# Kernel tuning notes

Measured on AMD Instinct MI355X. Metric: run time of the kernel, lower is better.

The kernel has to match this reference:

```python
import jax, jax.numpy as jnp
import numpy as np

N_NODES = 100000
N_EDGES = 1600000
D_IN = 128
D_HID = 128
D_OUT = 128
N_GRAPHS = 64


def setup_inputs() -> dict:
    key = jax.random.key(0)
    ks = jax.random.split(key, 10)
    x = jax.random.normal(ks[0], (N_NODES, D_IN), dtype=jnp.float32)
    edge_index = jax.random.randint(ks[1], (2, N_EDGES), 0, N_NODES, dtype=jnp.int64)
    graph_id = jnp.sort(jax.random.randint(ks[2], (N_NODES,), 0, N_GRAPHS, dtype=jnp.int64))
    s1 = 1.0 / np.sqrt(D_IN)
    s2 = 1.0 / np.sqrt(D_HID)
    s3 = 1.0 / np.sqrt(D_OUT)
    W1 = jax.random.normal(ks[3], (D_IN, D_HID), dtype=jnp.float32) * s1
    b1 = jnp.zeros((D_HID,), dtype=jnp.float32)
    W2 = jax.random.normal(ks[4], (D_HID, D_OUT), dtype=jnp.float32) * s2
    b2 = jnp.zeros((D_OUT,), dtype=jnp.float32)
    Wr1 = jax.random.normal(ks[5], (D_OUT, D_OUT), dtype=jnp.float32) * s3
    br1 = jnp.zeros((D_OUT,), dtype=jnp.float32)
    Wr2 = jax.random.normal(ks[6], (D_OUT, D_OUT), dtype=jnp.float32) * s3
    br2 = jnp.zeros((D_OUT,), dtype=jnp.float32)
    return {"x": x, "edge_index": edge_index, "graph_id": graph_id,
            "num_graphs": N_GRAPHS, "W1": W1, "b1": b1, "W2": W2, "b2": b2,
            "Wr1": Wr1, "br1": br1, "Wr2": Wr2, "br2": br2}


def _graph_conv(h, W, b, src, dst, norm_src, norm_dst, n_nodes):
    # DGL GraphConv, norm='both': out = D_dst^{-1/2} A (D_src^{-1/2} h) W + b
    h = h * norm_src[:, None]
    h = h @ W  # project first (cheap, keeps SpMM on the smaller/equal dim)
    agg = jax.ops.segment_sum(h[src], dst, num_segments=n_nodes)
    return agg * norm_dst[:, None] + b


def reference(x, edge_index, graph_id, num_graphs, W1, b1, W2, b2, Wr1, br1, Wr2, br2):
    src, dst = edge_index[0], edge_index[1]
    n_nodes = x.shape[0]
    ones = jnp.ones((src.shape[0],), dtype=x.dtype)
    deg_out = jax.ops.segment_sum(ones, src, num_segments=n_nodes)
    deg_in = jax.ops.segment_sum(ones, dst, num_segments=n_nodes)
    norm_src = jnp.clip(deg_out, 1.0) ** -0.5
    norm_dst = jnp.clip(deg_in, 1.0) ** -0.5

    # layer 1 + relu (dropout is identity in eval mode)
    h = _graph_conv(x, W1, b1, src, dst, norm_src, norm_dst, n_nodes)
    h = jax.nn.relu(h)
    # layer 2 + relu
    h = _graph_conv(h, W2, b2, src, dst, norm_src, norm_dst, n_nodes)
    h = jax.nn.relu(h)

    # per-graph mean pooling (dgl.mean_nodes)
    sums = jax.ops.segment_sum(h, graph_id, num_segments=num_graphs)
    counts = jax.ops.segment_sum(jnp.ones((n_nodes,), dtype=h.dtype), graph_id,
                                 num_segments=num_graphs)
    hg = sums / jnp.clip(counts, 1.0)[:, None]

    # readout MLP: Linear -> ReLU -> Linear
    out = jax.nn.relu(hg @ Wr1 + br1) @ Wr2 + br2
    return (out, h)
```

## Files before the change

### kernel.cpp

```cpp
#include <hip/hip_runtime.h>
#include <math.h>


#define D 128
#define BSH 8
#define BKT 256
#define CAP 4608
#define SCHUNK 3200

typedef _Float16 half8 __attribute__((ext_vector_type(8)));
typedef _Float16 half4v __attribute__((ext_vector_type(4)));
typedef _Float16 half2v __attribute__((ext_vector_type(2)));
typedef float f32x4 __attribute__((ext_vector_type(4)));

union H8 { half8 v; half2v h[4]; };

__global__ __launch_bounds__(512) void k_build(const int* __restrict__ src,
                                               const int* __restrict__ dst,
                                               int* __restrict__ cnt_d,
                                               int* __restrict__ cnt_s,
                                               int* __restrict__ packed_d,
                                               unsigned char* __restrict__ packed_s8,
                                               const float* __restrict__ W1,
                                               const float* __restrict__ W2,
                                               _Float16* __restrict__ Wt1,
                                               _Float16* __restrict__ Wt2,
                                               const int* __restrict__ gid,
                                               int* __restrict__ gptr,
                                               int N, int E, int nbkt) {
  __shared__ int hd[512], hs[512], exd[512], exs[512], based[512], bases[512];
  __shared__ int sd[SCHUNK];
  __shared__ unsigned char ss[SCHUNK];
  const int t = threadIdx.x;
  const int bid = blockIdx.x;

  for (int idx = bid * 512 + t; idx < 2 * 128 * 128; idx += gridDim.x * 512) {
    int m = idx >> 14, i = idx & 16383;
    int k = i >> 7, n = i & 127;
    (m ? Wt2 : Wt1)[n * 128 + k] = (_Float16)((m ? W2 : W1)[i]);
  }
  if (bid == gridDim.x - 1 && t <= 64) {
    int lo = 0, hi = N;
    while (lo < hi) {
      int m = (lo + hi) >> 1;
      if (gid[m] < t) lo = m + 1; else hi = m;
    }
    gptr[t] = lo;
  }

  hd[t] = 0; hs[t] = 0;
  __syncthreads();
  const int chunk = (E + gridDim.x - 1) / gridDim.x;
  const int lo = bid * chunk, hi = min(lo + chunk, E);
  const int n = hi - lo;
  for (int i = lo + t; i < hi; i += 512) {
    atomicAdd(&hd[dst[i] >> BSH], 1);
    atomicAdd(&hs[src[i] >> BSH], 1);
  }
  __syncthreads();
  int cD = hd[t], cS = hs[t];
  for (int off = 1; off < 512; off <<= 1) {
    int ad = (t >= off) ? hd[t - off] : 0;
    int as = (t >= off) ? hs[t - off] : 0;
    __syncthreads();
    hd[t] += ad; hs[t] += as;
    __syncthreads();
  }
  exd[t] = hd[t] - cD;
  exs[t] = hs[t] - cS;
  if (t < nbkt) {
    based[t] = cD ? atomicAdd(&cnt_d[t], cD) : 0;
    bases[t] = cS ? atomicAdd(&cnt_s[t], cS) : 0;
  }
  __syncthreads();
  hd[t] = 0; hs[t] = 0;
  __syncthreads();
  for (int i = lo + t; i < hi; i += 512) {
    int s = src[i], d = dst[i];
    int b1 = d >> BSH;
    int r1 = atomicAdd(&hd[b1], 1);
    sd[exd[b1] + r1] = ((d & (BKT - 1)) << 17) | s;
    int b2 = s >> BSH;
    int r2 = atomicAdd(&hs[b2], 1);
    ss[exs[b2] + r2] = (unsigned char)(s & (BKT - 1));
  }
  __syncthreads();
  for (int i = t; i < n; i += 512) {
    int blo = 0, bhi = nbkt - 1;
    while (blo < bhi) {
      int m = (blo + bhi + 1) >> 1;
      if (exd[m] <= i) blo = m; else bhi = m - 1;
    }
    int p = based[blo] + (i - exd[blo]);
    if (p < CAP) packed_d[blo * CAP + p] = sd[i];
    blo = 0; bhi = nbkt - 1;
    while (blo < bhi) {
      int m = (blo + bhi + 1) >> 1;
      if (exs[m] <= i) blo = m; else bhi = m - 1;
    }
    p = bases[blo] + (i - exs[blo]);
    if (p < CAP) packed_s8[blo * CAP + p] = ss[i];
  }
}

union FineLds {
  struct { int excl[256]; int ecache[CAP]; int sorted[CAP]; } d;
  struct { _Float16 As[64][136]; _Float16 Cs[64][128]; } s;
};

__global__ __launch_bounds__(512) void k_fine(const int* __restrict__ packed_d,
                                              const int* __restrict__ cnt_d,
                                              int* __restrict__ row_lo,
                                              int* __restrict__ row_hi,
                                              int* __restrict__ csr,
                                              const unsigned char* __restrict__ packed_s8,
                                              const int* __restrict__ cnt_s,
                                              float* __restrict__ norm_src,
                                              const float* __restrict__ x,
                                              const _Float16* __restrict__ Wt1,
                                              _Float16* __restrict__ P,
                                              int N, int nbkt) {
  __shared__ int hist[256];
  __shared__ FineLds u;
  int t = threadIdx.x;
  if (blockIdx.x >= nbkt) {
    int b = blockIdx.x - nbkt;
    size_t lo = (size_t)b * CAP;
    int cnt = min(cnt_s[b], CAP);
    if (t < 256) hist[t] = 0;
    __syncthreads();
    for (int e = t; e < cnt; e += 512)
      atomicAdd(&hist[packed_s8[lo + e]], 1);
    __syncthreads();
    int nbase = b << BSH;
    if (t < 256 && nbase + t < N)
      norm_src[nbase + t] = rsqrtf(fmaxf((float)hist[t], 1.0f));
    __syncthreads();
    const int l = t & 63;
    const int c = l & 15, quad = l >> 4;
    const int w = t >> 6;
    const int strip = w & 3, chalf = w >> 2;
    for (int ti = 0; ti < 4; ++ti) {
      const int r0 = nbase + ti * 64;
      for (int i = t; i < 64 * 32; i += 512) {
        int r = i >> 5, c4 = i & 31;
        float4 v = {0.f, 0.f, 0.f, 0.f};
        if (r0 + r < N) {
          v = ((const float4*)x)[(size_t)(r0 + r) * 32 + c4];
          float s = rsqrtf(fmaxf((float)hist[ti * 64 + r], 1.0f));
          v.x *= s; v.y *= s; v.z *= s; v.w *= s;
        }
        half4v h = {(_Float16)v.x, (_Float16)v.y, (_Float16)v.z, (_Float16)v.w};
        *(half4v*)&u.s.As[r][c4 * 4] = h;
      }
      __syncthreads();
      f32x4 acc[4];
#pragma unroll
      for (int nt = 0; nt < 4; ++nt) acc[nt] = (f32x4){0.f, 0.f, 0.f, 0.f};
#pragma unroll
      for (int kc = 0; kc < 4; ++kc) {
        half8 a = *(const half8*)&u.s.As[strip * 16 + c][kc * 32 + quad * 8];
#pragma unroll
        for (int nt = 0; nt < 4; ++nt) {
          half8 bb = *(const half8*)&Wt1[(size_t)(chalf * 64 + nt * 16 + c) * 128 + kc * 32 + quad * 8];
          acc[nt] = __builtin_amdgcn_mfma_f32_16x16x32_f16(a, bb, acc[nt], 0, 0, 0);
        }
      }
#pragma unroll
      for (int nt = 0; nt < 4; ++nt)
#pragma unroll
        for (int r = 0; r < 4; ++r)
          u.s.Cs[strip * 16 + quad * 4 + r][chalf * 64 + nt * 16 + c] = (_Float16)acc[nt][r];
      __syncthreads();
      for (int i = t; i < 64 * 16; i += 512) {
        int r = i >> 4, c8 = i & 15;
        if (r0 + r < N)
          ((half8*)P)[(size_t)(r0 + r) * 16 + c8] = *(half8*)&u.s.Cs[r][c8 * 8];
      }
      __syncthreads();
    }
    return;
  }
  int b = blockIdx.x;
  int lo = b * CAP;
  int cnt = min(cnt_d[b], CAP);
  if (t < 256) hist[t] = 0;
  __syncthreads();
  for (int e = t; e < cnt; e += 512) {
    int p = packed_d[lo + e];
    u.d.ecache[e] = p;
    atomicAdd(&hist[p >> 17], 1);
  }
  __syncthreads();
  int v = (t < 256) ? hist[t] : 0;
  for (int off = 1; off < 256; off <<= 1) {
    int a = (t >= off && t < 256) ? hist[t - off] : 0;
    __syncthreads();
    if (t < 256) hist[t] += a;
    __syncthreads();
  }
  int nbase = b << BSH;
  if (t < 256) {
    u.d.excl[t] = hist[t] - v;
    if (nbase + t < N) {
      row_lo[nbase + t] = lo + hist[t] - v;
      row_hi[nbase + t] = lo + hist[t];
    }
  }
  __syncthreads();
  if (t < 256) hist[t] = 0;
  __syncthreads();
  for (int e = t; e < cnt; e += 512) {
    int p = u.d.ecache[e];
    int dlow = p >> 17;
    int r = atomicAdd(&hist[dlow], 1);
    u.d.sorted[u.d.excl[dlow] + r] = p & 0x1FFFF;
  }
  __syncthreads();
  for (int e = t; e < cnt; e += 512)
    csr[lo + e] = u.d.sorted[e];
}

__global__ __launch_bounds__(256) void k_gemm2(const _Float16* __restrict__ A,
                                               const _Float16* __restrict__ Wt,
                                               _Float16* __restrict__ C, int N) {
  __shared__ _Float16 As[64][136];
  __shared__ _Float16 Cs[64][128];
  const int r0 = blockIdx.x * 64;
  const int t = threadIdx.x;
  for (int i = t; i < 64 * 16; i += 256) {
    int r = i >> 4, c8 = i & 15;
    half8 v = {0, 0, 0, 0, 0, 0, 0, 0};
    if (r0 + r < N) v = ((const half8*)A)[(size_t)(r0 + r) * 16 + c8];
    *(half8*)&As[r][c8 * 8] = v;
  }
  __syncthreads();
  const int w = t >> 6, l = t & 63;
  const int c = l & 15, quad = l >> 4;
  f32x4 acc[8];
#pragma unroll
  for (int nt = 0; nt < 8; ++nt) acc[nt] = (f32x4){0.f, 0.f, 0.f, 0.f};
#pragma unroll
  for (int kc = 0; kc < 4; ++kc) {
    half8 a = *(const half8*)&As[w * 16 + c][kc * 32 + quad * 8];
#pragma unroll
    for (int nt = 0; nt < 8; ++nt) {
      half8 b = *(const half8*)&Wt[(size_t)(nt * 16 + c) * 128 + kc * 32 + quad * 8];
      acc[nt] = __builtin_amdgcn_mfma_f32_16x16x32_f16(a, b, acc[nt], 0, 0, 0);
    }
  }
#pragma unroll
  for (int nt = 0; nt < 8; ++nt)
#pragma unroll
    for (int r = 0; r < 4; ++r)
      Cs[w * 16 + quad * 4 + r][nt * 16 + c] = (_Float16)acc[nt][r];
  __syncthreads();
  for (int i = t; i < 64 * 16; i += 256) {
    int r = i >> 4, c8 = i & 15;
    if (r0 + r < N)
      ((half8*)C)[(size_t)(r0 + r) * 16 + c8] = *(half8*)&Cs[r][c8 * 8];
  }
}

#define PK_ROW(u)                                                           \
  _Pragma("unroll")                                                         \
  for (int k = 0; k < 4; ++k) acch[k] += (u).h[k];

__device__ __forceinline__ void gather_core(const half8* __restrict__ P8,
                                            const int* __restrict__ csr,
                                            int start, int end, int cg, int eg,
                                            int lane, float* acc) {
  half2v acch[4] = {{(_Float16)0.f, (_Float16)0.f}, {(_Float16)0.f, (_Float16)0.f},
                    {(_Float16)0.f, (_Float16)0.f}, {(_Float16)0.f, (_Float16)0.f}};
  for (int s0 = start; s0 < end; s0 += 64) {
    int cnt = min(64, end - s0);
    int idx = (s0 + lane < end) ? csr[s0 + lane] : 0;
    int base = 0;
    for (; base + 16 <= cnt; base += 16) {
      int i0 = __shfl(idx, base + eg);
      int i1 = __shfl(idx, base + 4 + eg);
      int i2 = __shfl(idx, base + 8 + eg);
      int i3 = __shfl(idx, base + 12 + eg);
      H8 u0, u1, u2, u3;
      u0.v = P8[(size_t)i0 * 16 + cg];
      u1.v = P8[(size_t)i1 * 16 + cg];
      u2.v = P8[(size_t)i2 * 16 + cg];
      u3.v = P8[(size_t)i3 * 16 + cg];
      PK_ROW(u0) PK_ROW(u1) PK_ROW(u2) PK_ROW(u3)
    }
    for (; base + 4 <= cnt; base += 4) {
      int i0 = __shfl(idx, base + eg);
      H8 u0;
      u0.v = P8[(size_t)i0 * 16 + cg];
      PK_ROW(u0)
    }
    if (base < cnt) {
      int j = min(base + eg, cnt - 1);
      int i0 = __shfl(idx, j);
      if (base + eg < cnt) {
        H8 u0;
        u0.v = P8[(size_t)i0 * 16 + cg];
        PK_ROW(u0)
      }
    }
  }
#pragma unroll
  for (int k = 0; k < 4; ++k) {
    acc[2 * k]     = (float)acch[k].x;
    acc[2 * k + 1] = (float)acch[k].y;
  }
#pragma unroll
  for (int j = 0; j < 8; ++j) {
    acc[j] += __shfl_xor(acc[j], 16);
    acc[j] += __shfl_xor(acc[j], 32);
  }
}

__global__ __launch_bounds__(256) void k_gather1(const half8* __restrict__ P8,
                                                 const int* __restrict__ row_lo,
                                                 const int* __restrict__ row_hi,
                                                 const int* __restrict__ csr,
                                                 const float* __restrict__ bias,
                                                 const float* __restrict__ norm_src,
                                                 half2v* __restrict__ outH, int N) {
  int wid = (blockIdx.x * 256 + threadIdx.x) >> 6;
  if (wid >= N) return;
  int lane = threadIdx.x & 63;
  int cg = lane & 15, eg = lane >> 4;
  int start = row_lo[wid], end = row_hi[wid];
  float acc[8];
  gather_core(P8, csr, start, end, cg, eg, lane, acc);
  float nd = rsqrtf(fmaxf((float)(end - start), 1.0f));
  float ns = norm_src[wid];
  float2 b = ((const float2*)bias)[cg * 4 + eg];
  half2v o = {(_Float16)(fmaxf(acc[eg * 2] * nd + b.x, 0.f) * ns),
              (_Float16)(fmaxf(acc[eg * 2 + 1] * nd + b.y, 0.f) * ns)};
  outH[(size_t)wid * 64 + cg * 4 + eg] = o;
}

__global__ __launch_bounds__(256) void k_gather2(const half8* __restrict__ P8,
                                                 const int* __restrict__ row_lo,
                                                 const int* __restrict__ row_hi,
                                                 const int* __restrict__ csr,
                                                 const float* __restrict__ bias,
                                                 float2* __restrict__ outH, int N) {
  int wid = (blockIdx.x * 256 + threadIdx.x) >> 6;
  if (wid >= N) return;
  int lane = threadIdx.x & 63;
  int cg = lane & 15, eg = lane >> 4;
  int start = row_lo[wid], end = row_hi[wid];
  float acc[8];
  gather_core(P8, csr, start, end, cg, eg, lane, acc);
  float nd = rsqrtf(fmaxf((float)(end - start), 1.0f));
  float2 b = ((const float2*)bias)[cg * 4 + eg];
  float2 o;
  o.x = fmaxf(acc[eg * 2] * nd + b.x, 0.f);
  o.y = fmaxf(acc[eg * 2 + 1] * nd + b.y, 0.f);
  outH[(size_t)wid * 64 + cg * 4 + eg] = o;
}

__global__ __launch_bounds__(256) void k_pool(const float* __restrict__ H,
                                              const int* __restrict__ gptr,
                                              float* __restrict__ pool) {
  int g = blockIdx.x >> 3, chunk = blockIdx.x & 7;
  int col = threadIdx.x & 127, rpar = threadIdx.x >> 7;
  int s = gptr[g], e = gptr[g + 1];
  float acc = 0.0f;
  for (int r = s + chunk * 2 + rpar; r < e; r += 16)
    acc += H[(size_t)r * D + col];
  __shared__ float red[256];
  red[threadIdx.x] = acc;
  __syncthreads();
  if (rpar == 0) atomicAdd(&pool[g * D + col], acc + red[threadIdx.x + 128]);
}

__global__ __launch_bounds__(128) void k_readout(const float* __restrict__ pool,
                                                 const int* __restrict__ gptr,
                                                 const float* __restrict__ Wr1,
                                                 const float* __restrict__ br1,
                                                 const float* __restrict__ Wr2,
                                                 const float* __restrict__ br2,
                                                 float* __restrict__ out) {
  int g = blockIdx.x;
  int j = threadIdx.x;
  __shared__ float hg[D];
  __shared__ float t1[D];
  float cnt = fmaxf((float)(gptr[g + 1] - gptr[g]), 1.0f);
  hg[j] = pool[(size_t)g * D + j] / cnt;
  __syncthreads();
  float a = br1[j];
  for (int k = 0; k < D; ++k) a += hg[k] * Wr1[(size_t)k * D + j];
  t1[j] = fmaxf(a, 0.0f);
  __syncthreads();
  float b = br2[j];
  for (int k = 0; k < D; ++k) b += t1[k] * Wr2[(size_t)k * D + j];
  out[(size_t)g * D + j] = b;
}

extern "C" void kernel_launch(void* const* d_in, const int* in_sizes, int n_in,
                              void* d_out, int out_size, void* d_ws, size_t ws_size,
                              hipStream_t stream) {
  const float* x   = (const float*)d_in[0];
  const int* edge  = (const int*)d_in[1];
  const int* gid   = (const int*)d_in[2];
  const float* W1  = (const float*)d_in[4];
  const float* b1  = (const float*)d_in[5];
  const float* W2  = (const float*)d_in[6];
  const float* b2  = (const float*)d_in[7];
  const float* Wr1 = (const float*)d_in[8];
  const float* br1 = (const float*)d_in[9];
  const float* Wr2 = (const float*)d_in[10];
  const float* br2 = (const float*)d_in[11];

  const int N = in_sizes[0] / D;
  const int E = in_sizes[1] / 2;
  const int* src = edge;
  const int* dst = edge + E;
  const int nbkt = (N + BKT - 1) >> BSH;

  float* bufA     = (float*)d_ws;
  float* bufB     = bufA + (size_t)N * D;
  int* row_lo     = (int*)(bufB + (size_t)N * D);
  int* row_hi     = row_lo + N;
  int* csr        = row_hi + N;
  float* norm_src = (float*)(csr + (size_t)nbkt * CAP);
  float* pool     = norm_src + N;
  int* gptr       = (int*)(pool + 64 * D);
  int* cnt_d      = gptr + 65;
  int* cnt_s      = cnt_d + 512;
  _Float16* Wt1   = (_Float16*)(cnt_s + 512);
  _Float16* Wt2   = Wt1 + 128 * 128;
  int* packed_d   = (int*)(bufA + (size_t)N * D / 2);
  unsigned char* packed_s8 = (unsigned char*)(packed_d + (size_t)nbkt * CAP);
  size_t need = ((size_t)2 * N * D + 3 * (size_t)N + (size_t)nbkt * CAP
                 + 64 * D + 65 + 1024 + 16384 + 1024) * sizeof(float);
  if (ws_size < need) return;

  float* out_g = (float*)d_out;
  float* h_out = out_g + 64 * D;

  _Float16* P   = (_Float16*)bufA;
  _Float16* h1p = (_Float16*)bufB;

  hipMemsetAsync(pool, 0, (64 * D + 65 + 1024) * sizeof(float), stream);

  const int build_grid = (E + SCHUNK - 1) / SCHUNK;
  k_build<<<build_grid, 512, 0, stream>>>(src, dst, cnt_d, cnt_s,
                                          packed_d, packed_s8,
                                          W1, W2, Wt1, Wt2, gid, gptr,
                                          N, E, nbkt);
  k_fine<<<2 * nbkt, 512, 0, stream>>>(packed_d, cnt_d, row_lo, row_hi, csr,
                                       packed_s8, cnt_s, norm_src,
                                       x, Wt1, P, N, nbkt);

  k_gather1<<<(N * 64 + 255) / 256, 256, 0, stream>>>(
      (const half8*)P, row_lo, row_hi, csr, b1, norm_src, (half2v*)h1p, N);

  const int gemm_grid = (N + 63) / 64;
  k_gemm2<<<gemm_grid, 256, 0, stream>>>(h1p, Wt2, P, N);
  k_gather2<<<(N * 64 + 255) / 256, 256, 0, stream>>>(
      (const half8*)P, row_lo, row_hi, csr, b2, (float2*)h_out, N);

  k_pool<<<64 * 8, 256, 0, stream>>>(h_out, gptr, pool);
  k_readout<<<64, 128, 0, stream>>>(pool, gptr, Wr1, br1, Wr2, br2, out_g);
}
```

Measured before the change: 372.7 us.

## Fuse layer-1 gather with layer-2 GEMM into one kernel via shared memory

Merges the layer-1 SpMM gather kernel and the layer-2 dense projection GEMM. Each block gathers 32 rows (8 rows per wave, run one after another) into LDS and then multiplies them by W2 with MFMA, writing P2 directly. This removes the h1 round trip through global memory and one kernel launch. In exchange, each wave now handles 8 rows serially, and blocks holding high-degree rows are held back at the barrier, which can lower memory-level parallelism in the gather.

```diff
diff --git a/kernel.cpp b/kernel.cpp
--- a/kernel.cpp
+++ b/kernel.cpp
@@ -219,47 +219,6 @@
   __syncthreads();
   for (int e = t; e < cnt; e += 512)
     csr[lo + e] = u.d.sorted[e];
-}
-
-__global__ __launch_bounds__(256) void k_gemm2(const _Float16* __restrict__ A,
-                                               const _Float16* __restrict__ Wt,
-                                               _Float16* __restrict__ C, int N) {
-  __shared__ _Float16 As[64][136];
-  __shared__ _Float16 Cs[64][128];
-  const int r0 = blockIdx.x * 64;
-  const int t = threadIdx.x;
-  for (int i = t; i < 64 * 16; i += 256) {
-    int r = i >> 4, c8 = i & 15;
-    half8 v = {0, 0, 0, 0, 0, 0, 0, 0};
-    if (r0 + r < N) v = ((const half8*)A)[(size_t)(r0 + r) * 16 + c8];
-    *(half8*)&As[r][c8 * 8] = v;
-  }
-  __syncthreads();
-  const int w = t >> 6, l = t & 63;
-  const int c = l & 15, quad = l >> 4;
-  f32x4 acc[8];
-#pragma unroll
-  for (int nt = 0; nt < 8; ++nt) acc[nt] = (f32x4){0.f, 0.f, 0.f, 0.f};
-#pragma unroll
-  for (int kc = 0; kc < 4; ++kc) {
-    half8 a = *(const half8*)&As[w * 16 + c][kc * 32 + quad * 8];
-#pragma unroll
-    for (int nt = 0; nt < 8; ++nt) {
-      half8 b = *(const half8*)&Wt[(size_t)(nt * 16 + c) * 128 + kc * 32 + quad * 8];
-      acc[nt] = __builtin_amdgcn_mfma_f32_16x16x32_f16(a, b, acc[nt], 0, 0, 0);
-    }
-  }
-#pragma unroll
-  for (int nt = 0; nt < 8; ++nt)
-#pragma unroll
-    for (int r = 0; r < 4; ++r)
-      Cs[w * 16 + quad * 4 + r][nt * 16 + c] = (_Float16)acc[nt][r];
-  __syncthreads();
-  for (int i = t; i < 64 * 16; i += 256) {
-    int r = i >> 4, c8 = i & 15;
-    if (r0 + r < N)
-      ((half8*)C)[(size_t)(r0 + r) * 16 + c8] = *(half8*)&Cs[r][c8 * 8];
-  }
 }
 
 #define PK_ROW(u)                                                           \
@@ -316,26 +275,62 @@
   }
 }
 
-__global__ __launch_bounds__(256) void k_gather1(const half8* __restrict__ P8,
-                                                 const int* __restrict__ row_lo,
-                                                 const int* __restrict__ row_hi,
-                                                 const int* __restrict__ csr,
-                                                 const float* __restrict__ bias,
-                                                 const float* __restrict__ norm_src,
-                                                 half2v* __restrict__ outH, int N) {
-  int wid = (blockIdx.x * 256 + threadIdx.x) >> 6;
-  if (wid >= N) return;
-  int lane = threadIdx.x & 63;
-  int cg = lane & 15, eg = lane >> 4;
-  int start = row_lo[wid], end = row_hi[wid];
-  float acc[8];
-  gather_core(P8, csr, start, end, cg, eg, lane, acc);
-  float nd = rsqrtf(fmaxf((float)(end - start), 1.0f));
-  float ns = norm_src[wid];
+__global__ __launch_bounds__(256) void k_g1g2(const half8* __restrict__ P8,
+                                              const int* __restrict__ row_lo,
+                                              const int* __restrict__ row_hi,
+                                              const int* __restrict__ csr,
+                                              const float* __restrict__ bias,
+                                              const float* __restrict__ norm_src,
+                                              const _Float16* __restrict__ Wt2,
+                                              _Float16* __restrict__ P2, int N) {
+  __shared__ _Float16 As[32][136];
+  __shared__ _Float16 Cs[32][128];
+  const int t = threadIdx.x;
+  const int w = t >> 6, lane = t & 63;
+  const int cg = lane & 15, eg = lane >> 4;
+  const int r0 = blockIdx.x * 32;
   float2 b = ((const float2*)bias)[cg * 4 + eg];
-  half2v o = {(_Float16)(fmaxf(acc[eg * 2] * nd + b.x, 0.f) * ns),
-              (_Float16)(fmaxf(acc[eg * 2 + 1] * nd + b.y, 0.f) * ns)};
-  outH[(size_t)wid * 64 + cg * 4 + eg] = o;
+  for (int j = 0; j < 8; ++j) {
+    int row = w * 8 + j;
+    int wid = r0 + row;
+    half2v o = {(_Float16)0.f, (_Float16)0.f};
+    if (wid < N) {
+      int start = row_lo[wid], end = row_hi[wid];
+      float acc[8];
+      gather_core(P8, csr, start, end, cg, eg, lane, acc);
+      float nd = rsqrtf(fmaxf((float)(end - start), 1.0f));
+      float ns = norm_src[wid];
+      o.x = (_Float16)(fmaxf(acc[eg * 2] * nd + b.x, 0.f) * ns);
+      o.y = (_Float16)(fmaxf(acc[eg * 2 + 1] * nd + b.y, 0.f) * ns);
+    }
+    *(half2v*)&As[row][2 * (cg * 4 + eg)] = o;
+  }
+  __syncthreads();
+  const int strip = w >> 1, chalf = w & 1;
+  const int c = cg, quad = eg;
+  f32x4 acc[4];
+#pragma unroll
+  for (int nt = 0; nt < 4; ++nt) acc[nt] = (f32x4){0.f, 0.f, 0.f, 0.f};
+#pragma unroll
+  for (int kc = 0; kc < 4; ++kc) {
+    half8 a = *(const half8*)&As[strip * 16 + c][kc * 32 + quad * 8];
+#pragma unroll
+    for (int nt = 0; nt < 4; ++nt) {
+      half8 bb = *(const half8*)&Wt2[(size_t)(chalf * 64 + nt * 16 + c) * 128 + kc * 32 + quad * 8];
+      acc[nt] = __builtin_amdgcn_mfma_f32_16x16x32_f16(a, bb, acc[nt], 0, 0, 0);
+    }
+  }
+#pragma unroll
+  for (int nt = 0; nt < 4; ++nt)
+#pragma unroll
+    for (int r = 0; r < 4; ++r)
+      Cs[strip * 16 + quad * 4 + r][chalf * 64 + nt * 16 + c] = (_Float16)acc[nt][r];
+  __syncthreads();
+  for (int i = t; i < 32 * 16; i += 256) {
+    int r = i >> 4, c8 = i & 15;
+    if (r0 + r < N)
+      ((half8*)P2)[(size_t)(r0 + r) * 16 + c8] = *(half8*)&Cs[r][c8 * 8];
+  }
 }
 
 __global__ __launch_bounds__(256) void k_gather2(const half8* __restrict__ P8,
@@ -439,8 +434,8 @@
   float* out_g = (float*)d_out;
   float* h_out = out_g + 64 * D;
 
-  _Float16* P   = (_Float16*)bufA;
-  _Float16* h1p = (_Float16*)bufB;
+  _Float16* P  = (_Float16*)bufA;
+  _Float16* P2 = (_Float16*)bufB;
 
   hipMemsetAsync(pool, 0, (64 * D + 65 + 1024) * sizeof(float), stream);
 
@@ -453,13 +448,11 @@
                                        packed_s8, cnt_s, norm_src,
                                        x, Wt1, P, N, nbkt);
 
-  k_gather1<<<(N * 64 + 255) / 256, 256, 0, stream>>>(
-      (const half8*)P, row_lo, row_hi, csr, b1, norm_src, (half2v*)h1p, N);
-
-  const int gemm_grid = (N + 63) / 64;
-  k_gemm2<<<gemm_grid, 256, 0, stream>>>(h1p, Wt2, P, N);
+  k_g1g2<<<(N + 31) / 32, 256, 0, stream>>>(
+      (const half8*)P, row_lo, row_hi, csr, b1, norm_src, Wt2, P2, N);
+
   k_gather2<<<(N * 64 + 255) / 256, 256, 0, stream>>>(
-      (const half8*)P, row_lo, row_hi, csr, b2, (float2*)h_out, N);
+      (const half8*)P2, row_lo, row_hi, csr, b2, (float2*)h_out, N);
 
   k_pool<<<64 * 8, 256, 0, stream>>>(h_out, gptr, pool);
   k_readout<<<64, 128, 0, stream>>>(pool, gptr, Wr1, br1, Wr2, br2, out_g);
```

Result: no change. 368.2 us (-1.2%).
